# Optimization experiments

Hardware: AMD Instinct MI355X
Metric: run time of the kernel (lower is better)

The kernel has to match this reference:

```python
import jax, jax.numpy as jnp
import numpy as np

EPS = 1e-5

def _layernorm(x, g, b):
    # normalize over last (channel) axis
    mu = jnp.mean(x, axis=-1, keepdims=True)
    var = jnp.var(x, axis=-1, keepdims=True)
    return (x - mu) * jax.lax.rsqrt(var + EPS) * g + b

def _dynamix(xt, wnd, bnd, wnn, bnn):
    # xt: [B, M, N, C]; mixes over the N axis (vectorized form of the per-slice loop)
    B, M, N, C = xt.shape
    d = wnd.shape[1]
    p = xt @ wnd + bnd                       # [B,M,N,d]
    p = p.reshape(B, M, N * d) @ wnn + bnn   # [B,M,N*N]
    p = jax.nn.softmax(p.reshape(B, M, N, N), axis=-1)
    return jnp.einsum('bmij,bmjc->bmic', p, xt)  # [B,M,N,C]

def setup_inputs() -> dict:
    key = jax.random.key(0)
    ks = jax.random.split(key, 10)
    B, C, H, W, d, E = 32, 128, 56, 56, 10, 4
    def n(k, shape, scale=0.02):
        return jax.random.normal(k, shape, jnp.float32) * scale
    return {
        'x': jax.random.normal(ks[0], (B, C, H, W), jnp.float32),
        'ln1_g': jnp.ones((C,), jnp.float32), 'ln1_b': jnp.zeros((C,), jnp.float32),
        'h_wnd': n(ks[1], (C, d)), 'h_bnd': jnp.zeros((d,), jnp.float32),
        'h_wnn': n(ks[2], (W * d, W * W)), 'h_bnn': jnp.zeros((W * W,), jnp.float32),
        'w_wnd': n(ks[3], (C, d)), 'w_bnd': jnp.zeros((d,), jnp.float32),
        'w_wnn': n(ks[4], (H * d, H * H)), 'w_bnn': jnp.zeros((H * H,), jnp.float32),
        'pc_w': n(ks[5], (C, C)), 'pc_b': jnp.zeros((C,), jnp.float32),
        'po_w': n(ks[6], (C, C)), 'po_b': jnp.zeros((C,), jnp.float32),
        'ln2_g': jnp.ones((C,), jnp.float32), 'ln2_b': jnp.zeros((C,), jnp.float32),
        'fc1_w': n(ks[7], (C, E * C)), 'fc1_b': jnp.zeros((E * C,), jnp.float32),
        'fc2_w': n(ks[8], (E * C, C)), 'fc2_b': jnp.zeros((C,), jnp.float32),
    }

def reference(x, ln1_g, ln1_b, h_wnd, h_bnd, h_wnn, h_bnn,
              w_wnd, w_bnd, w_wnn, w_bnn, pc_w, pc_b, po_w, po_b,
              ln2_g, ln2_b, fc1_w, fc1_b, fc2_w, fc2_b):
    # x: [B,C,H,W] -> work channels-last [B,H,W,C]
    xt = jnp.transpose(x, (0, 2, 3, 1))
    # ---- block p1: LN + DynaMixer ----
    u = _layernorm(xt, ln1_g, ln1_b)                 # [B,H,W,C]
    y_h = _dynamix(u, h_wnd, h_bnd, h_wnn, h_bnn)    # mix over W per row
    u_w = jnp.transpose(u, (0, 2, 1, 3))             # [B,W,H,C]
    y_w = _dynamix(u_w, w_wnd, w_bnd, w_wnn, w_bnn)  # mix over H per col
    y_w = jnp.transpose(y_w, (0, 2, 1, 3))           # back to [B,H,W,C]
    y_c = u @ pc_w + pc_b                            # 1x1 conv proj_c
    y = (y_h + y_w + y_c) @ po_w + po_b              # 1x1 conv proj_o
    xt = xt + y                                      # residual (drop_path=0)
    # ---- block p2: LN + MLP ----
    v = _layernorm(xt, ln2_g, ln2_b)
    h = jax.nn.gelu(v @ fc1_w + fc1_b, approximate=False)
    h = h @ fc2_w + fc2_b
    xt = xt + h
    return jnp.transpose(xt, (0, 3, 1, 2))           # [B,C,H,W]
```

## Files before the change

kernel.cpp:

```cpp
#include <hip/hip_runtime.h>
#include <math.h>

#define BB 32
#define CC 128
#define HH 56
#define WW 56
#define HWHW 3136
#define TOK 100352
#define TOKH 50176
#define BH 1792
#define NDP 576
#define NNP 3200

typedef __attribute__((ext_vector_type(8))) short bhalf8;
typedef __attribute__((ext_vector_type(4))) float f32x4;
typedef __attribute__((ext_vector_type(4))) unsigned int u32x4;

__device__ inline unsigned short f2bf(float f) {
  unsigned int x = __float_as_uint(f);
  unsigned int r = (x + 0x7FFFu + ((x >> 16) & 1u)) >> 16;
  return (unsigned short)r;
}
__device__ inline float bf2f(unsigned short u) {
  return __uint_as_float(((unsigned int)u) << 16);
}
__device__ inline unsigned int pack2(float a, float b) {
  return (unsigned int)f2bf(a) | ((unsigned int)f2bf(b) << 16);
}
__device__ inline f32x4 MFMA(bhalf8 a, bhalf8 b, f32x4 c) {
  return __builtin_amdgcn_mfma_f32_16x16x32_bf16(a, b, c, 0, 0, 0);
}
template <int CH>
__device__ inline bhalf8 ldsFrag(const unsigned short* base, int row, int chunk) {
  return *reinterpret_cast<const bhalf8*>(base + row * (CH * 8) + ((chunk ^ (row & 7)) * 8));
}
__device__ inline bhalf8 gFrag(const unsigned short* p) {
  return *reinterpret_cast<const bhalf8*>(p);
}
__device__ inline float gelu_f(float x) {
  float x3 = x * x * x;
  float z = 0.7978845608028654f * (x + 0.044715f * x3);
  float e = __expf(2.0f * z);
  float t = 1.0f - 2.0f / (e + 1.0f);
  return 0.5f * x * (1.0f + t);
}

__global__ __launch_bounds__(256) void wcvt_kernel(
    const float* __restrict__ hwnd, const float* __restrict__ wwnd,
    unsigned short* __restrict__ wcatT, u32x4* __restrict__ pdzero) {
  int gt = blockIdx.x * 256 + threadIdx.x;
  int gs = gridDim.x * 256;
  for (int i = gt; i < 258048; i += gs) { u32x4 z = {0, 0, 0, 0}; pdzero[i] = z; }
  for (int i = gt; i < 128 * 32; i += gs) {
    int k = i >> 5, n = i & 31;
    float v = n < 10 ? hwnd[k * 10 + n] : (n < 20 ? wwnd[k * 10 + (n - 10)] : 0.f);
    wcatT[n * 128 + k] = f2bf(v);
  }
}

__global__ __launch_bounds__(256) void wtrans_kernel(
    const float* __restrict__ hwnn, const float* __restrict__ wwnn,
    const float* __restrict__ pcw, const float* __restrict__ pow_,
    const float* __restrict__ fc1w, const float* __restrict__ fc2w,
    unsigned short* __restrict__ wnnTh, unsigned short* __restrict__ wnnTw,
    unsigned short* __restrict__ pcT, unsigned short* __restrict__ poT,
    unsigned short* __restrict__ fc1T, unsigned short* __restrict__ fc2T) {
  __shared__ unsigned short t[64][65];
  int bid = blockIdx.x;
  const float* src; unsigned short* dst;
  int K, N, Kp, Np, bx, by;
  if (bid < 450)      { src = hwnn; dst = wnnTh; K = 560; N = 3136; Kp = 576; Np = 3200; int b = bid;       bx = b % 50; by = b / 50; }
  else if (bid < 900) { src = wwnn; dst = wnnTw; K = 560; N = 3136; Kp = 576; Np = 3200; int b = bid - 450; bx = b % 50; by = b / 50; }
  else if (bid < 904) { src = pcw;  dst = pcT;   K = 128; N = 128;  Kp = 128; Np = 128;  int b = bid - 900; bx = b % 2;  by = b / 2; }
  else if (bid < 908) { src = pow_; dst = poT;   K = 128; N = 128;  Kp = 128; Np = 128;  int b = bid - 904; bx = b % 2;  by = b / 2; }
  else if (bid < 924) { src = fc1w; dst = fc1T;  K = 128; N = 512;  Kp = 128; Np = 512;  int b = bid - 908; bx = b % 8;  by = b / 8; }
  else                { src = fc2w; dst = fc2T;  K = 512; N = 128;  Kp = 512; Np = 128;  int b = bid - 924; bx = b % 2;  by = b / 2; }
  int n0 = bx * 64, k0 = by * 64;
  int tid = threadIdx.x;
  for (int idx = tid; idx < 4096; idx += 256) {
    int kk = idx >> 6, nn = idx & 63;
    float v = (k0 + kk < K && n0 + nn < N) ? src[(size_t)(k0 + kk) * N + n0 + nn] : 0.f;
    t[nn][kk] = f2bf(v);
  }
  __syncthreads();
  for (int idx = tid; idx < 4096; idx += 256) {
    int nn = idx >> 6, kk = idx & 63;
    if (n0 + nn < Np && k0 + kk < Kp)
      dst[(size_t)(n0 + nn) * Kp + k0 + kk] = t[nn][kk];
  }
}

__global__ __launch_bounds__(256) void ln1_kernel(const float* __restrict__ x,
    const float* __restrict__ g, const float* __restrict__ bt,
    unsigned short* __restrict__ ubf, unsigned short* __restrict__ xcl) {
  int bh = blockIdx.x;
  int b = bh / HH, h = bh % HH;
  __shared__ float lds[WW][CC + 1];
  __shared__ float mu[WW], rs[WW];
  const float* xp = x + ((size_t)b * CC) * HWHW + (size_t)h * WW;
  for (int idx = threadIdx.x; idx < CC * WW; idx += 256) {
    int c = idx / WW, w = idx % WW;
    lds[w][c] = xp[(size_t)c * HWHW + w];
  }
  __syncthreads();
  if (threadIdx.x < WW) {
    int w = threadIdx.x;
    float s = 0.f, ss = 0.f;
    for (int c = 0; c < CC; ++c) { float v = lds[w][c]; s += v; ss += v * v; }
    float m = s * (1.0f / CC);
    float var = ss * (1.0f / CC) - m * m;
    mu[w] = m; rs[w] = rsqrtf(var + 1e-5f);
  }
  __syncthreads();
  unsigned short* up = ubf + (size_t)bh * (WW * CC);
  unsigned short* xc = xcl + (size_t)bh * (WW * CC);
  for (int idx = threadIdx.x; idx < WW * CC; idx += 256) {
    int w = idx >> 7, c = idx & 127;
    float v = lds[w][c];
    up[idx] = f2bf((v - mu[w]) * rs[w] * g[c] + bt[c]);
    xc[idx] = f2bf(v);
  }
}

__global__ __launch_bounds__(256) void pd_mfma(const unsigned short* __restrict__ ubf,
    const unsigned short* __restrict__ wcatT, const float* __restrict__ hbnd,
    const float* __restrict__ wbnd, unsigned short* __restrict__ pdh,
    unsigned short* __restrict__ pdw) {
  __shared__ __align__(16) unsigned short sU[64 * 128];
  __shared__ __align__(16) unsigned short sW[32 * 128];
  int tid = threadIdx.x;
  int tok0 = blockIdx.x * 64;
  #pragma unroll
  for (int i = 0; i < 4; ++i) {
    int s = i * 256 + tid; int r = s >> 4, c = s & 15;
    u32x4 v = *reinterpret_cast<const u32x4*>(ubf + (size_t)(tok0 + r) * 128 + c * 8);
    *reinterpret_cast<u32x4*>(sU + r * 128 + ((c ^ (r & 7)) * 8)) = v;
  }
  #pragma unroll
  for (int i = 0; i < 2; ++i) {
    int s = i * 256 + tid; int r = s >> 4, c = s & 15;
    u32x4 v = *reinterpret_cast<const u32x4*>(wcatT + (size_t)r * 128 + c * 8);
    *reinterpret_cast<u32x4*>(sW + r * 128 + ((c ^ (r & 7)) * 8)) = v;
  }
  __syncthreads();
  int wid = tid >> 6, lane = tid & 63, l16 = lane & 15, lk = lane >> 4;
  f32x4 acc[2] = {};
  #pragma unroll
  for (int kk = 0; kk < 4; ++kk) {
    bhalf8 a = ldsFrag<16>(sU, wid * 16 + l16, kk * 4 + lk);
    #pragma unroll
    for (int f = 0; f < 2; ++f) {
      bhalf8 b = ldsFrag<16>(sW, f * 16 + l16, kk * 4 + lk);
      acc[f] = MFMA(a, b, acc[f]);
    }
  }
  #pragma unroll
  for (int f = 0; f < 2; ++f) {
    int n = f * 16 + l16;
    #pragma unroll
    for (int r = 0; r < 4; ++r) {
      int tok = tok0 + wid * 16 + lk * 4 + r;
      float v = acc[f][r];
      if (n < 10) {
        pdh[((size_t)(tok / 56)) * NDP + (size_t)(tok % 56) * 10 + n] = f2bf(v + hbnd[n]);
      } else if (n < 20) {
        int b = tok / HWHW; int rem = tok % HWHW; int hh = rem / 56; int w = rem % 56;
        pdw[((size_t)(b * 56 + w)) * NDP + (size_t)hh * 10 + (n - 10)] = f2bf(v + wbnd[n - 10]);
      }
    }
  }
}

__global__ __launch_bounds__(256) void gemm_logits(
    const unsigned short* __restrict__ A, const unsigned short* __restrict__ BT,
    const float* __restrict__ bias, unsigned short* __restrict__ Cout) {
  __shared__ __align__(16) unsigned short sA[128 * 64];
  __shared__ __align__(16) unsigned short sB[128 * 64];
  int tid = threadIdx.x;
  int row0 = blockIdx.y * 128, col0 = blockIdx.x * 128;
  int wid = tid >> 6, lane = tid & 63;
  int wm = wid >> 1, wn = wid & 1;
  int l16 = lane & 15, lk = lane >> 4;
  f32x4 acc[4][4] = {};
  for (int k0 = 0; k0 < NDP; k0 += 64) {
    #pragma unroll
    for (int i = 0; i < 4; ++i) {
      int s = i * 256 + tid; int r = s >> 3, c = s & 7;
      u32x4 v = *reinterpret_cast<const u32x4*>(A + (size_t)(row0 + r) * NDP + k0 + c * 8);
      *reinterpret_cast<u32x4*>(sA + r * 64 + ((c ^ (r & 7)) * 8)) = v;
    }
    #pragma unroll
    for (int i = 0; i < 4; ++i) {
      int s = i * 256 + tid; int r = s >> 3, c = s & 7;
      u32x4 v = *reinterpret_cast<const u32x4*>(BT + (size_t)(col0 + r) * NDP + k0 + c * 8);
      *reinterpret_cast<u32x4*>(sB + r * 64 + ((c ^ (r & 7)) * 8)) = v;
    }
    __syncthreads();
    bhalf8 af[4][2], bf[4][2];
    #pragma unroll
    for (int f = 0; f < 4; ++f)
      #pragma unroll
      for (int kk = 0; kk < 2; ++kk) {
        af[f][kk] = ldsFrag<8>(sA, wm * 64 + f * 16 + l16, kk * 4 + lk);
        bf[f][kk] = ldsFrag<8>(sB, wn * 64 + f * 16 + l16, kk * 4 + lk);
      }
    #pragma unroll
    for (int i = 0; i < 4; ++i)
      #pragma unroll
      for (int j = 0; j < 4; ++j) {
        acc[i][j] = MFMA(af[i][0], bf[j][0], acc[i][j]);
        acc[i][j] = MFMA(af[i][1], bf[j][1], acc[i][j]);
      }
    __syncthreads();
  }
  #pragma unroll
  for (int i = 0; i < 4; ++i) {
    int rbase = row0 + wm * 64 + i * 16 + lk * 4;
    #pragma unroll
    for (int j = 0; j < 4; ++j) {
      int col = col0 + wn * 64 + j * 16 + l16;
      if (col < HWHW) {
        float bv = bias[col];
        #pragma unroll
        for (int r = 0; r < 4; ++r)
          Cout[(size_t)(rbase + r) * NNP + col] = f2bf(acc[i][j][r] + bv);
      }
    }
  }
}

__global__ __launch_bounds__(256) void softmax56_kernel(unsigned short* __restrict__ ph,
                                                        unsigned short* __restrict__ pw) {
  int wave = (blockIdx.x * 256 + threadIdx.x) >> 6;
  int lane = threadIdx.x & 63;
  if (wave >= 2 * TOK) return;
  unsigned short* buf = wave < TOK ? ph : pw;
  int row = wave < TOK ? wave : wave - TOK;
  int bh = row / 56, i = row % 56;
  unsigned short* p = buf + (size_t)bh * NNP + (size_t)i * 56;
  float xv = lane < WW ? bf2f(p[lane]) : -INFINITY;
  float m = xv;
  for (int o = 32; o > 0; o >>= 1) m = fmaxf(m, __shfl_xor(m, o));
  float e = lane < WW ? __expf(xv - m) : 0.f;
  float s = e;
  for (int o = 32; o > 0; o >>= 1) s += __shfl_xor(s, o);
  if (lane < WW) p[lane] = f2bf(e / s);
}

__global__ __launch_bounds__(256) void mixh_pc(const unsigned short* __restrict__ ph,
    const unsigned short* __restrict__ ubf, const unsigned short* __restrict__ pcT,
    const float* __restrict__ pcb, unsigned short* __restrict__ accm) {
  int bh = blockIdx.x;
  int tok0 = bh * 56;
  __shared__ __align__(16) unsigned short sUt[128 * 64];
  int tid = threadIdx.x;
  for (int s = tid; s < 1024; s += 256) {
    int j = s >> 4, cc = s & 15;
    unsigned short e8[8] = {0, 0, 0, 0, 0, 0, 0, 0};
    if (j < 56)
      *reinterpret_cast<u32x4*>(e8) =
          *reinterpret_cast<const u32x4*>(ubf + (size_t)(tok0 + j) * 128 + cc * 8);
    #pragma unroll
    for (int e = 0; e < 8; ++e) {
      int cf = cc * 8 + e;
      sUt[cf * 64 + (((j >> 3) ^ (cf & 7)) * 8) + (j & 7)] = e8[e];
    }
  }
  __syncthreads();
  int lane = tid & 63, l16 = lane & 15, lk = lane >> 4, wn = tid >> 6;
  const unsigned short* prow = ph + (size_t)bh * NNP;
  f32x4 acc[4][2] = {};
  #pragma unroll
  for (int kk = 0; kk < 2; ++kk) {
    bhalf8 a[4], b[2];
    #pragma unroll
    for (int i = 0; i < 4; ++i)
      a[i] = gFrag(prow + (i * 16 + l16) * 56 + (kk * 4 + lk) * 8);
    #pragma unroll
    for (int j = 0; j < 2; ++j) b[j] = ldsFrag<8>(sUt, wn * 32 + j * 16 + l16, kk * 4 + lk);
    #pragma unroll
    for (int i = 0; i < 4; ++i)
      #pragma unroll
      for (int j = 0; j < 2; ++j) acc[i][j] = MFMA(a[i], b[j], acc[i][j]);
  }
  #pragma unroll
  for (int kk = 0; kk < 4; ++kk) {
    bhalf8 a[4], b[2];
    #pragma unroll
    for (int i = 0; i < 4; ++i)
      a[i] = gFrag(ubf + (size_t)(tok0 + i * 16 + l16) * 128 + (kk * 4 + lk) * 8);
    #pragma unroll
    for (int j = 0; j < 2; ++j)
      b[j] = gFrag(pcT + (size_t)(wn * 32 + j * 16 + l16) * 128 + (kk * 4 + lk) * 8);
    #pragma unroll
    for (int i = 0; i < 4; ++i)
      #pragma unroll
      for (int j = 0; j < 2; ++j) acc[i][j] = MFMA(a[i], b[j], acc[i][j]);
  }
  #pragma unroll
  for (int i = 0; i < 4; ++i) {
    int tok = i * 16 + lk * 4;
    #pragma unroll
    for (int j = 0; j < 2; ++j) {
      int c = wn * 32 + j * 16 + l16;
      float bv = pcb[c];
      #pragma unroll
      for (int r = 0; r < 4; ++r)
        if (tok + r < 56)
          accm[(size_t)(tok0 + tok + r) * 128 + c] = f2bf(acc[i][j][r] + bv);
    }
  }
}

__global__ __launch_bounds__(256) void mixw_fin(const unsigned short* __restrict__ pw,
    const unsigned short* __restrict__ ubf, const unsigned short* __restrict__ poT,
    const float* __restrict__ pob, const unsigned short* __restrict__ xcl,
    unsigned short* __restrict__ accXt) {
  int bw = blockIdx.x;
  int bq = bw / 56, w = bw % 56;
  __shared__ __align__(16) unsigned short sUt[128 * 64];
  __shared__ __align__(16) unsigned short sS[64 * 128];
  int tid = threadIdx.x;
  for (int s = tid; s < 1024; s += 256) {
    int j = s >> 4, cc = s & 15;
    unsigned short e8[8] = {0, 0, 0, 0, 0, 0, 0, 0};
    if (j < 56)
      *reinterpret_cast<u32x4*>(e8) =
          *reinterpret_cast<const u32x4*>(ubf + ((size_t)bq * HWHW + (size_t)j * 56 + w) * 128 + cc * 8);
    #pragma unroll
    for (int e = 0; e < 8; ++e) {
      int cf = cc * 8 + e;
      sUt[cf * 64 + (((j >> 3) ^ (cf & 7)) * 8) + (j & 7)] = e8[e];
    }
  }
  for (int s = tid; s < 1024; s += 256) {
    int r = s >> 4, c = s & 15;
    u32x4 v = {0, 0, 0, 0};
    if (r < 56) v = *reinterpret_cast<const u32x4*>(accXt + ((size_t)bq * HWHW + (size_t)r * 56 + w) * 128 + c * 8);
    *reinterpret_cast<u32x4*>(sS + r * 128 + ((c ^ (r & 7)) * 8)) = v;
  }
  __syncthreads();
  int lane = tid & 63, l16 = lane & 15, lk = lane >> 4, wn = tid >> 6;
  const unsigned short* prow = pw + (size_t)bw * NNP;
  f32x4 acc1[4][2] = {};
  #pragma unroll
  for (int kk = 0; kk < 2; ++kk) {
    bhalf8 a[4], b[2];
    #pragma unroll
    for (int i = 0; i < 4; ++i)
      a[i] = gFrag(prow + (i * 16 + l16) * 56 + (kk * 4 + lk) * 8);
    #pragma unroll
    for (int j = 0; j < 2; ++j) b[j] = ldsFrag<8>(sUt, wn * 32 + j * 16 + l16, kk * 4 + lk);
    #pragma unroll
    for (int i = 0; i < 4; ++i)
      #pragma unroll
      for (int j = 0; j < 2; ++j) acc1[i][j] = MFMA(a[i], b[j], acc1[i][j]);
  }
  __syncthreads();
  #pragma unroll
  for (int i = 0; i < 4; ++i) {
    #pragma unroll
    for (int j = 0; j < 2; ++j) {
      int col = wn * 32 + j * 16 + l16;
      #pragma unroll
      for (int r = 0; r < 4; ++r) {
        int row = i * 16 + lk * 4 + r;
        int ad = row * 128 + (((col >> 3) ^ (row & 7)) * 8) + (col & 7);
        sS[ad] = f2bf(bf2f(sS[ad]) + acc1[i][j][r]);
      }
    }
  }
  __syncthreads();
  f32x4 acc2[4][2] = {};
  #pragma unroll
  for (int kk = 0; kk < 4; ++kk) {
    bhalf8 a[4], b[2];
    #pragma unroll
    for (int i = 0; i < 4; ++i) a[i] = ldsFrag<16>(sS, i * 16 + l16, kk * 4 + lk);
    #pragma unroll
    for (int j = 0; j < 2; ++j)
      b[j] = gFrag(poT + (size_t)(wn * 32 + j * 16 + l16) * 128 + (kk * 4 + lk) * 8);
    #pragma unroll
    for (int i = 0; i < 4; ++i)
      #pragma unroll
      for (int j = 0; j < 2; ++j) acc2[i][j] = MFMA(a[i], b[j], acc2[i][j]);
  }
  #pragma unroll
  for (int i = 0; i < 4; ++i) {
    #pragma unroll
    for (int j = 0; j < 2; ++j) {
      int c = wn * 32 + j * 16 + l16;
      float bv = pob[c];
      #pragma unroll
      for (int r = 0; r < 4; ++r) {
        int row = i * 16 + lk * 4 + r;
        if (row < 56) {
          size_t t = (size_t)bq * HWHW + (size_t)row * 56 + w;
          float z = acc2[i][j][r] + bv + bf2f(xcl[t * 128 + c]);
          accXt[t * 128 + c] = f2bf(z);
        }
      }
    }
  }
}

__global__ __launch_bounds__(256) void ln2_kernel(const unsigned short* __restrict__ xt2,
    const float* __restrict__ g, const float* __restrict__ bt,
    unsigned short* __restrict__ vbf) {
  int wave = (blockIdx.x * 256 + threadIdx.x) >> 6;
  int lane = threadIdx.x & 63;
  if (wave >= TOK) return;
  const unsigned short* xp = xt2 + (size_t)wave * CC;
  unsigned int wrd = *reinterpret_cast<const unsigned int*>(xp + lane * 2);
  float a = bf2f((unsigned short)(wrd & 0xFFFFu));
  float b2v = bf2f((unsigned short)(wrd >> 16));
  float s = a + b2v, ss = a * a + b2v * b2v;
  for (int o = 32; o > 0; o >>= 1) { s += __shfl_xor(s, o); ss += __shfl_xor(ss, o); }
  float m = s * (1.0f / CC);
  float var = ss * (1.0f / CC) - m * m;
  float rv = rsqrtf(var + 1e-5f);
  int c0 = lane * 2;
  float n0 = (a - m) * rv * g[c0] + bt[c0];
  float n1 = (b2v - m) * rv * g[c0 + 1] + bt[c0 + 1];
  *reinterpret_cast<unsigned int*>(vbf + (size_t)wave * CC + c0) = pack2(n0, n1);
}

__global__ __launch_bounds__(256) void gemm_fc1(const unsigned short* __restrict__ vbf,
    const unsigned short* __restrict__ fc1T, const float* __restrict__ b1,
    unsigned short* __restrict__ hbuf, int tokOff) {
  __shared__ __align__(16) unsigned short sW[128 * 64];
  __shared__ __align__(16) unsigned short sV[128 * 64];
  __shared__ float b1s[128];
  int tid = threadIdx.x;
  int hidT = blockIdx.x * 128;
  int tok0 = blockIdx.y * 128;
  if (tid < 128) b1s[tid] = b1[hidT + tid];
  int wid = tid >> 6, lane = tid & 63;
  int wm = wid >> 1, wn = wid & 1;
  int l16 = lane & 15, lk = lane >> 4;
  f32x4 acc[4][4] = {};
  for (int k0 = 0; k0 < 128; k0 += 64) {
    #pragma unroll
    for (int i = 0; i < 4; ++i) {
      int s = i * 256 + tid; int r = s >> 3, c = s & 7;
      u32x4 v = *reinterpret_cast<const u32x4*>(fc1T + (size_t)(hidT + r) * 128 + k0 + c * 8);
      *reinterpret_cast<u32x4*>(sW + r * 64 + ((c ^ (r & 7)) * 8)) = v;
    }
    #pragma unroll
    for (int i = 0; i < 4; ++i) {
      int s = i * 256 + tid; int r = s >> 3, c = s & 7;
      u32x4 v = *reinterpret_cast<const u32x4*>(vbf + (size_t)(tokOff + tok0 + r) * 128 + k0 + c * 8);
      *reinterpret_cast<u32x4*>(sV + r * 64 + ((c ^ (r & 7)) * 8)) = v;
    }
    __syncthreads();
    bhalf8 af[4][2], bf[4][2];
    #pragma unroll
    for (int f = 0; f < 4; ++f)
      #pragma unroll
      for (int kk = 0; kk < 2; ++kk) {
        af[f][kk] = ldsFrag<8>(sW, wm * 64 + f * 16 + l16, kk * 4 + lk);
        bf[f][kk] = ldsFrag<8>(sV, wn * 64 + f * 16 + l16, kk * 4 + lk);
      }
    #pragma unroll
    for (int i = 0; i < 4; ++i)
      #pragma unroll
      for (int j = 0; j < 4; ++j) {
        acc[i][j] = MFMA(af[i][0], bf[j][0], acc[i][j]);
        acc[i][j] = MFMA(af[i][1], bf[j][1], acc[i][j]);
      }
    __syncthreads();
  }
  #pragma unroll
  for (int i = 0; i < 4; ++i) {
    int hidL = wm * 64 + i * 16 + lk * 4;
    #pragma unroll
    for (int j = 0; j < 4; ++j) {
      int tokL = wn * 64 + j * 16 + l16;
      float v0 = gelu_f(acc[i][j][0] + b1s[hidL]);
      float v1 = gelu_f(acc[i][j][1] + b1s[hidL + 1]);
      float v2 = gelu_f(acc[i][j][2] + b1s[hidL + 2]);
      float v3 = gelu_f(acc[i][j][3] + b1s[hidL + 3]);
      unsigned long long pk = (unsigned long long)pack2(v0, v1)
                            | ((unsigned long long)pack2(v2, v3) << 32);
      *reinterpret_cast<unsigned long long*>(
          hbuf + (size_t)(tok0 + tokL) * 512 + hidT + hidL) = pk;
    }
  }
}

__global__ __launch_bounds__(256) void gemm_fc2(const unsigned short* __restrict__ hbuf,
    const unsigned short* __restrict__ fc2T, const float* __restrict__ b2,
    const unsigned short* __restrict__ xt2, float* __restrict__ out, int tokOff) {
  __shared__ __align__(16) unsigned short smem[2][128 * 64];
  __shared__ float b2s[128];
  unsigned short* sH = smem[0];
  unsigned short* sC = smem[1];
  unsigned short* xtile = &smem[0][0];
  int tid = threadIdx.x;
  int tok0 = blockIdx.x * 128;
  if (tid < 128) b2s[tid] = b2[tid];
  int wid = tid >> 6, lane = tid & 63;
  int wm = wid >> 1, wn = wid & 1;
  int l16 = lane & 15, lk = lane >> 4;
  f32x4 acc[4][4] = {};
  for (int k0 = 0; k0 < 512; k0 += 64) {
    #pragma unroll
    for (int i = 0; i < 4; ++i) {
      int s = i * 256 + tid; int r = s >> 3, c = s & 7;
      u32x4 v = *reinterpret_cast<const u32x4*>(hbuf + (size_t)(tok0 + r) * 512 + k0 + c * 8);
      *reinterpret_cast<u32x4*>(sH + r * 64 + ((c ^ (r & 7)) * 8)) = v;
    }
    #pragma unroll
    for (int i = 0; i < 4; ++i) {
      int s = i * 256 + tid; int r = s >> 3, c = s & 7;
      u32x4 v = *reinterpret_cast<const u32x4*>(fc2T + (size_t)r * 512 + k0 + c * 8);
      *reinterpret_cast<u32x4*>(sC + r * 64 + ((c ^ (r & 7)) * 8)) = v;
    }
    __syncthreads();
    bhalf8 af[4][2], bf[4][2];
    #pragma unroll
    for (int f = 0; f < 4; ++f)
      #pragma unroll
      for (int kk = 0; kk < 2; ++kk) {
        af[f][kk] = ldsFrag<8>(sH, wm * 64 + f * 16 + l16, kk * 4 + lk);
        bf[f][kk] = ldsFrag<8>(sC, wn * 64 + f * 16 + l16, kk * 4 + lk);
      }
    #pragma unroll
    for (int i = 0; i < 4; ++i)
      #pragma unroll
      for (int j = 0; j < 4; ++j) {
        acc[i][j] = MFMA(af[i][0], bf[j][0], acc[i][j]);
        acc[i][j] = MFMA(af[i][1], bf[j][1], acc[i][j]);
      }
    __syncthreads();
  }
  #pragma unroll
  for (int i = 0; i < 8; ++i) {
    int s = i * 256 + tid; int r = s >> 4, c = s & 15;
    u32x4 v = *reinterpret_cast<const u32x4*>(xt2 + (size_t)(tokOff + tok0 + r) * 128 + c * 8);
    *reinterpret_cast<u32x4*>(xtile + r * 128 + c * 8) = v;
  }
  __syncthreads();
  #pragma unroll
  for (int i = 0; i < 4; ++i) {
    int tokL = wm * 64 + i * 16 + lk * 4;
    int tokG = tokOff + tok0 + tokL;
    int bqv = tokG / HWHW;
    int pos = tokG - bqv * HWHW;
    #pragma unroll
    for (int j = 0; j < 4; ++j) {
      int cL = wn * 64 + j * 16 + l16;
      float bv = b2s[cL];
      f32x4 o;
      #pragma unroll
      for (int r = 0; r < 4; ++r)
        o[r] = acc[i][j][r] + bv + bf2f(xtile[(tokL + r) * 128 + cL]);
      *reinterpret_cast<f32x4*>(out + ((size_t)(bqv * CC + cL)) * HWHW + pos) = o;
    }
  }
}

extern "C" void kernel_launch(void* const* d_in, const int* in_sizes, int n_in,
                              void* d_out, int out_size, void* d_ws, size_t ws_size,
                              hipStream_t stream) {
  const float* x     = (const float*)d_in[0];
  const float* ln1_g = (const float*)d_in[1];
  const float* ln1_b = (const float*)d_in[2];
  const float* h_wnd = (const float*)d_in[3];
  const float* h_bnd = (const float*)d_in[4];
  const float* h_wnn = (const float*)d_in[5];
  const float* h_bnn = (const float*)d_in[6];
  const float* w_wnd = (const float*)d_in[7];
  const float* w_bnd = (const float*)d_in[8];
  const float* w_wnn = (const float*)d_in[9];
  const float* w_bnn = (const float*)d_in[10];
  const float* pc_w  = (const float*)d_in[11];
  const float* pc_b  = (const float*)d_in[12];
  const float* po_w  = (const float*)d_in[13];
  const float* po_b  = (const float*)d_in[14];
  const float* ln2_g = (const float*)d_in[15];
  const float* ln2_b = (const float*)d_in[16];
  const float* fc1_w = (const float*)d_in[17];
  const float* fc1_b = (const float*)d_in[18];
  const float* fc2_w = (const float*)d_in[19];
  const float* fc2_b = (const float*)d_in[20];
  float* out = (float*)d_out;
  char* ws = (char*)d_ws;

  unsigned short* ubf   = (unsigned short*)(ws + 0);
  unsigned short* xcl   = (unsigned short*)(ws + 25690112);
  unsigned short* accXt = (unsigned short*)(ws + 51380224);
  unsigned short* pdh   = (unsigned short*)(ws + 77070336);
  unsigned short* pdw   = (unsigned short*)(ws + 79134720);
  unsigned short* ph    = (unsigned short*)(ws + 81199104);
  unsigned short* pw    = (unsigned short*)(ws + 92667904);
  unsigned short* wnnTh = (unsigned short*)(ws + 104136704);
  unsigned short* wnnTw = (unsigned short*)(ws + 107823104);
  unsigned short* hhalf = (unsigned short*)(ws + 77070336);
  unsigned short* pcT   = (unsigned short*)(ws + 128450560);
  unsigned short* poT   = (unsigned short*)(ws + 128483328);
  unsigned short* fc1T  = (unsigned short*)(ws + 128516096);
  unsigned short* fc2T  = (unsigned short*)(ws + 128647168);
  unsigned short* wcatT = (unsigned short*)(ws + 128778240);
  unsigned short* vbf   = ubf;

  wcvt_kernel<<<1008, 256, 0, stream>>>(h_wnd, w_wnd, wcatT, (u32x4*)pdh);
  wtrans_kernel<<<940, 256, 0, stream>>>(h_wnn, w_wnn, pc_w, po_w, fc1_w, fc2_w,
      wnnTh, wnnTw, pcT, poT, fc1T, fc2T);
  ln1_kernel<<<BH, 256, 0, stream>>>(x, ln1_g, ln1_b, ubf, xcl);
  pd_mfma<<<TOK / 64, 256, 0, stream>>>(ubf, wcatT, h_bnd, w_bnd, pdh, pdw);
  gemm_logits<<<dim3(NNP / 128, BH / 128), 256, 0, stream>>>(pdh, wnnTh, h_bnn, ph);
  gemm_logits<<<dim3(NNP / 128, BH / 128), 256, 0, stream>>>(pdw, wnnTw, w_bnn, pw);
  softmax56_kernel<<<(2 * TOK) / 4, 256, 0, stream>>>(ph, pw);
  mixh_pc<<<BH, 256, 0, stream>>>(ph, ubf, pcT, pc_b, accXt);
  mixw_fin<<<BB * WW, 256, 0, stream>>>(pw, ubf, poT, po_b, xcl, accXt);
  ln2_kernel<<<TOK / 4, 256, 0, stream>>>(accXt, ln2_g, ln2_b, vbf);
  gemm_fc1<<<dim3(4, TOKH / 128), 256, 0, stream>>>(vbf, fc1T, fc1_b, hhalf, 0);
  gemm_fc2<<<TOKH / 128, 256, 0, stream>>>(hhalf, fc2T, fc2_b, accXt, out, 0);
  gemm_fc1<<<dim3(4, TOKH / 128), 256, 0, stream>>>(vbf, fc1T, fc1_b, hhalf, TOKH);
  gemm_fc2<<<TOKH / 128, 256, 0, stream>>>(hhalf, fc2T, fc2_b, accXt, out, TOKH);
}
```

Measured before the change: 307.0 us.

## Merge prep and logits launches, fuse LN2 into mixw, unsplit MLP GEMMs

Folds the weight-convert/zero kernel into the weight-transpose launch and merges the two logits GEMMs into one grid, so fewer launches run. LayerNorm2 is fused into the mixw_fin epilogue by staging the residual tile in shared memory, which removes a separate pass over the activations. The fc1/fc2 GEMMs now run once over all tokens using a full-size hidden buffer, with the weight buffers relocated to make room. The cost is a much larger workspace footprint and extra shared-memory traffic and barriers in mixw_fin.

Measured after the change: 287.2 us, median of 2. 1.07x faster.

```diff
diff --git a/kernel.cpp b/kernel.cpp
--- a/kernel.cpp
+++ b/kernel.cpp
@@ -7,7 +7,6 @@
 #define WW 56
 #define HWHW 3136
 #define TOK 100352
-#define TOKH 50176
 #define BH 1792
 #define NDP 576
 #define NNP 3200
@@ -45,28 +44,28 @@
   return 0.5f * x * (1.0f + t);
 }
 
-__global__ __launch_bounds__(256) void wcvt_kernel(
-    const float* __restrict__ hwnd, const float* __restrict__ wwnd,
-    unsigned short* __restrict__ wcatT, u32x4* __restrict__ pdzero) {
-  int gt = blockIdx.x * 256 + threadIdx.x;
-  int gs = gridDim.x * 256;
-  for (int i = gt; i < 258048; i += gs) { u32x4 z = {0, 0, 0, 0}; pdzero[i] = z; }
-  for (int i = gt; i < 128 * 32; i += gs) {
-    int k = i >> 5, n = i & 31;
-    float v = n < 10 ? hwnd[k * 10 + n] : (n < 20 ? wwnd[k * 10 + (n - 10)] : 0.f);
-    wcatT[n * 128 + k] = f2bf(v);
-  }
-}
-
 __global__ __launch_bounds__(256) void wtrans_kernel(
     const float* __restrict__ hwnn, const float* __restrict__ wwnn,
     const float* __restrict__ pcw, const float* __restrict__ pow_,
     const float* __restrict__ fc1w, const float* __restrict__ fc2w,
+    const float* __restrict__ hwnd, const float* __restrict__ wwnd,
     unsigned short* __restrict__ wnnTh, unsigned short* __restrict__ wnnTw,
     unsigned short* __restrict__ pcT, unsigned short* __restrict__ poT,
-    unsigned short* __restrict__ fc1T, unsigned short* __restrict__ fc2T) {
+    unsigned short* __restrict__ fc1T, unsigned short* __restrict__ fc2T,
+    unsigned short* __restrict__ wcatT, u32x4* __restrict__ pdzero) {
   __shared__ unsigned short t[64][65];
   int bid = blockIdx.x;
+  int tid = threadIdx.x;
+  if (bid >= 940) {
+    int gt = (bid - 940) * 256 + tid, gs = 64 * 256;
+    for (int i = gt; i < 258048; i += gs) { u32x4 z = {0, 0, 0, 0}; pdzero[i] = z; }
+    for (int i = gt; i < 128 * 32; i += gs) {
+      int k = i >> 5, n = i & 31;
+      float v = n < 10 ? hwnd[k * 10 + n] : (n < 20 ? wwnd[k * 10 + (n - 10)] : 0.f);
+      wcatT[n * 128 + k] = f2bf(v);
+    }
+    return;
+  }
   const float* src; unsigned short* dst;
   int K, N, Kp, Np, bx, by;
   if (bid < 450)      { src = hwnn; dst = wnnTh; K = 560; N = 3136; Kp = 576; Np = 3200; int b = bid;       bx = b % 50; by = b / 50; }
@@ -76,7 +75,6 @@
   else if (bid < 924) { src = fc1w; dst = fc1T;  K = 128; N = 512;  Kp = 128; Np = 512;  int b = bid - 908; bx = b % 8;  by = b / 8; }
   else                { src = fc2w; dst = fc2T;  K = 512; N = 128;  Kp = 512; Np = 128;  int b = bid - 924; bx = b % 2;  by = b / 2; }
   int n0 = bx * 64, k0 = by * 64;
-  int tid = threadIdx.x;
   for (int idx = tid; idx < 4096; idx += 256) {
     int kk = idx >> 6, nn = idx & 63;
     float v = (k0 + kk < K && n0 + nn < N) ? src[(size_t)(k0 + kk) * N + n0 + nn] : 0.f;
@@ -172,12 +170,19 @@
 }
 
 __global__ __launch_bounds__(256) void gemm_logits(
-    const unsigned short* __restrict__ A, const unsigned short* __restrict__ BT,
-    const float* __restrict__ bias, unsigned short* __restrict__ Cout) {
+    const unsigned short* __restrict__ pdh, const unsigned short* __restrict__ pdw,
+    const unsigned short* __restrict__ wnnTh, const unsigned short* __restrict__ wnnTw,
+    const float* __restrict__ hbnn, const float* __restrict__ wbnn,
+    unsigned short* __restrict__ ph, unsigned short* __restrict__ pwb) {
   __shared__ __align__(16) unsigned short sA[128 * 64];
   __shared__ __align__(16) unsigned short sB[128 * 64];
   int tid = threadIdx.x;
-  int row0 = blockIdx.y * 128, col0 = blockIdx.x * 128;
+  int byr = blockIdx.y;
+  const unsigned short* A; const unsigned short* BT; const float* bias; unsigned short* Cout;
+  int row0;
+  if (byr < 14) { A = pdh; BT = wnnTh; bias = hbnn; Cout = ph;  row0 = byr * 128; }
+  else          { A = pdw; BT = wnnTw; bias = wbnn; Cout = pwb; row0 = (byr - 14) * 128; }
+  int col0 = blockIdx.x * 128;
   int wid = tid >> 6, lane = tid & 63;
   int wm = wid >> 1, wn = wid & 1;
   int l16 = lane & 15, lk = lane >> 4;
@@ -315,7 +320,9 @@
 __global__ __launch_bounds__(256) void mixw_fin(const unsigned short* __restrict__ pw,
     const unsigned short* __restrict__ ubf, const unsigned short* __restrict__ poT,
     const float* __restrict__ pob, const unsigned short* __restrict__ xcl,
-    unsigned short* __restrict__ accXt) {
+    unsigned short* __restrict__ accXt,
+    const float* __restrict__ ln2g, const float* __restrict__ ln2b,
+    unsigned short* __restrict__ vbf) {
   int bw = blockIdx.x;
   int bq = bw / 56, w = bw % 56;
   __shared__ __align__(16) unsigned short sUt[128 * 64];
@@ -385,6 +392,7 @@
       #pragma unroll
       for (int j = 0; j < 2; ++j) acc2[i][j] = MFMA(a[i], b[j], acc2[i][j]);
   }
+  __syncthreads();
   #pragma unroll
   for (int i = 0; i < 4; ++i) {
     #pragma unroll
@@ -397,37 +405,40 @@
         if (row < 56) {
           size_t t = (size_t)bq * HWHW + (size_t)row * 56 + w;
           float z = acc2[i][j][r] + bv + bf2f(xcl[t * 128 + c]);
-          accXt[t * 128 + c] = f2bf(z);
+          unsigned short zb = f2bf(z);
+          accXt[t * 128 + c] = zb;
+          sS[row * 128 + (((c >> 3) ^ (row & 7)) * 8) + (c & 7)] = zb;
         }
       }
     }
   }
-}
-
-__global__ __launch_bounds__(256) void ln2_kernel(const unsigned short* __restrict__ xt2,
-    const float* __restrict__ g, const float* __restrict__ bt,
-    unsigned short* __restrict__ vbf) {
-  int wave = (blockIdx.x * 256 + threadIdx.x) >> 6;
-  int lane = threadIdx.x & 63;
-  if (wave >= TOK) return;
-  const unsigned short* xp = xt2 + (size_t)wave * CC;
-  unsigned int wrd = *reinterpret_cast<const unsigned int*>(xp + lane * 2);
-  float a = bf2f((unsigned short)(wrd & 0xFFFFu));
-  float b2v = bf2f((unsigned short)(wrd >> 16));
-  float s = a + b2v, ss = a * a + b2v * b2v;
-  for (int o = 32; o > 0; o >>= 1) { s += __shfl_xor(s, o); ss += __shfl_xor(ss, o); }
-  float m = s * (1.0f / CC);
-  float var = ss * (1.0f / CC) - m * m;
-  float rv = rsqrtf(var + 1e-5f);
-  int c0 = lane * 2;
-  float n0 = (a - m) * rv * g[c0] + bt[c0];
-  float n1 = (b2v - m) * rv * g[c0 + 1] + bt[c0 + 1];
-  *reinterpret_cast<unsigned int*>(vbf + (size_t)wave * CC + c0) = pack2(n0, n1);
+  __syncthreads();
+  {
+    int wid4 = tid >> 6;
+    int c0 = 2 * lane;
+    float g0 = ln2g[c0], g1 = ln2g[c0 + 1];
+    float b0 = ln2b[c0], b1 = ln2b[c0 + 1];
+    for (int row = wid4; row < 56; row += 4) {
+      int ad = row * 128 + (((c0 >> 3) ^ (row & 7)) * 8) + (c0 & 7);
+      unsigned int wrd = *reinterpret_cast<const unsigned int*>(sS + ad);
+      float z0 = bf2f((unsigned short)(wrd & 0xFFFFu));
+      float z1 = bf2f((unsigned short)(wrd >> 16));
+      float s1 = z0 + z1, s2 = z0 * z0 + z1 * z1;
+      for (int o = 32; o > 0; o >>= 1) { s1 += __shfl_xor(s1, o); s2 += __shfl_xor(s2, o); }
+      float m = s1 * (1.0f / CC);
+      float var = s2 * (1.0f / CC) - m * m;
+      float rv = rsqrtf(var + 1e-5f);
+      float n0 = (z0 - m) * rv * g0 + b0;
+      float n1 = (z1 - m) * rv * g1 + b1;
+      size_t t = (size_t)bq * HWHW + (size_t)row * 56 + w;
+      *reinterpret_cast<unsigned int*>(vbf + t * 128 + c0) = pack2(n0, n1);
+    }
+  }
 }
 
 __global__ __launch_bounds__(256) void gemm_fc1(const unsigned short* __restrict__ vbf,
     const unsigned short* __restrict__ fc1T, const float* __restrict__ b1,
-    unsigned short* __restrict__ hbuf, int tokOff) {
+    unsigned short* __restrict__ hbuf) {
   __shared__ __align__(16) unsigned short sW[128 * 64];
   __shared__ __align__(16) unsigned short sV[128 * 64];
   __shared__ float b1s[128];
@@ -449,7 +460,7 @@
     #pragma unroll
     for (int i = 0; i < 4; ++i) {
       int s = i * 256 + tid; int r = s >> 3, c = s & 7;
-      u32x4 v = *reinterpret_cast<const u32x4*>(vbf + (size_t)(tokOff + tok0 + r) * 128 + k0 + c * 8);
+      u32x4 v = *reinterpret_cast<const u32x4*>(vbf + (size_t)(tok0 + r) * 128 + k0 + c * 8);
       *reinterpret_cast<u32x4*>(sV + r * 64 + ((c ^ (r & 7)) * 8)) = v;
     }
     __syncthreads();
@@ -490,7 +501,7 @@
 
 __global__ __launch_bounds__(256) void gemm_fc2(const unsigned short* __restrict__ hbuf,
     const unsigned short* __restrict__ fc2T, const float* __restrict__ b2,
-    const unsigned short* __restrict__ xt2, float* __restrict__ out, int tokOff) {
+    const unsigned short* __restrict__ xt2, float* __restrict__ out) {
   __shared__ __align__(16) unsigned short smem[2][128 * 64];
   __shared__ float b2s[128];
   unsigned short* sH = smem[0];
@@ -537,14 +548,14 @@
   #pragma unroll
   for (int i = 0; i < 8; ++i) {
     int s = i * 256 + tid; int r = s >> 4, c = s & 15;
-    u32x4 v = *reinterpret_cast<const u32x4*>(xt2 + (size_t)(tokOff + tok0 + r) * 128 + c * 8);
+    u32x4 v = *reinterpret_cast<const u32x4*>(xt2 + (size_t)(tok0 + r) * 128 + c * 8);
     *reinterpret_cast<u32x4*>(xtile + r * 128 + c * 8) = v;
   }
   __syncthreads();
   #pragma unroll
   for (int i = 0; i < 4; ++i) {
     int tokL = wm * 64 + i * 16 + lk * 4;
-    int tokG = tokOff + tok0 + tokL;
+    int tokG = tok0 + tokL;
     int bqv = tokG / HWHW;
     int pos = tokG - bqv * HWHW;
     #pragma unroll
@@ -596,27 +607,24 @@
   unsigned short* pw    = (unsigned short*)(ws + 92667904);
   unsigned short* wnnTh = (unsigned short*)(ws + 104136704);
   unsigned short* wnnTw = (unsigned short*)(ws + 107823104);
-  unsigned short* hhalf = (unsigned short*)(ws + 77070336);
-  unsigned short* pcT   = (unsigned short*)(ws + 128450560);
-  unsigned short* poT   = (unsigned short*)(ws + 128483328);
-  unsigned short* fc1T  = (unsigned short*)(ws + 128516096);
-  unsigned short* fc2T  = (unsigned short*)(ws + 128647168);
-  unsigned short* wcatT = (unsigned short*)(ws + 128778240);
+  unsigned short* hbuf  = (unsigned short*)(ws + 77070336);
+  unsigned short* pcT   = (unsigned short*)(ws + 179830784);
+  unsigned short* poT   = (unsigned short*)(ws + 179863552);
+  unsigned short* fc1T  = (unsigned short*)(ws + 179896320);
+  unsigned short* fc2T  = (unsigned short*)(ws + 180027392);
+  unsigned short* wcatT = (unsigned short*)(ws + 180158464);
   unsigned short* vbf   = ubf;
 
-  wcvt_kernel<<<1008, 256, 0, stream>>>(h_wnd, w_wnd, wcatT, (u32x4*)pdh);
-  wtrans_kernel<<<940, 256, 0, stream>>>(h_wnn, w_wnn, pc_w, po_w, fc1_w, fc2_w,
-      wnnTh, wnnTw, pcT, poT, fc1T, fc2T);
+  wtrans_kernel<<<1004, 256, 0, stream>>>(h_wnn, w_wnn, pc_w, po_w, fc1_w, fc2_w,
+      h_wnd, w_wnd, wnnTh, wnnTw, pcT, poT, fc1T, fc2T, wcatT, (u32x4*)pdh);
   ln1_kernel<<<BH, 256, 0, stream>>>(x, ln1_g, ln1_b, ubf, xcl);
   pd_mfma<<<TOK / 64, 256, 0, stream>>>(ubf, wcatT, h_bnd, w_bnd, pdh, pdw);
-  gemm_logits<<<dim3(NNP / 128, BH / 128), 256, 0, stream>>>(pdh, wnnTh, h_bnn, ph);
-  gemm_logits<<<dim3(NNP / 128, BH / 128), 256, 0, stream>>>(pdw, wnnTw, w_bnn, pw);
+  gemm_logits<<<dim3(NNP / 128, 28), 256, 0, stream>>>(pdh, pdw, wnnTh, wnnTw,
+      h_bnn, w_bnn, ph, pw);
   softmax56_kernel<<<(2 * TOK) / 4, 256, 0, stream>>>(ph, pw);
   mixh_pc<<<BH, 256, 0, stream>>>(ph, ubf, pcT, pc_b, accXt);
-  mixw_fin<<<BB * WW, 256, 0, stream>>>(pw, ubf, poT, po_b, xcl, accXt);
-  ln2_kernel<<<TOK / 4, 256, 0, stream>>>(accXt, ln2_g, ln2_b, vbf);
-  gemm_fc1<<<dim3(4, TOKH / 128), 256, 0, stream>>>(vbf, fc1T, fc1_b, hhalf, 0);
-  gemm_fc2<<<TOKH / 128, 256, 0, stream>>>(hhalf, fc2T, fc2_b, accXt, out, 0);
-  gemm_fc1<<<dim3(4, TOKH / 128), 256, 0, stream>>>(vbf, fc1T, fc1_b, hhalf, TOKH);
-  gemm_fc2<<<TOKH / 128, 256, 0, stream>>>(hhalf, fc2T, fc2_b, accXt, out, TOKH);
-}
+  mixw_fin<<<BB * WW, 256, 0, stream>>>(pw, ubf, poT, po_b, xcl, accXt,
+      ln2_g, ln2_b, vbf);
+  gemm_fc1<<<dim3(4, TOK / 128), 256, 0, stream>>>(vbf, fc1T, fc1_b, hbuf);
+  gemm_fc2<<<TOK / 128, 256, 0, stream>>>(hbuf, fc2T, fc2_b, accXt, out);
+}
```
